# Kernel optimization log

Hardware: AMD Instinct MI355X
Metric: run time of the kernel (lower is better)

Reference implementation:

```python
import jax, jax.numpy as jnp
import numpy as np

SIGMA = 2.0
B, F, N = 4, 64, 4096


def setup_inputs() -> dict:
    key = jax.random.key(0)
    emb_in = jax.random.normal(key, (B, F, N), dtype=jnp.float32)
    adj_in = jnp.zeros((B, N, N), dtype=jnp.float32)  # unused by the module, kept for interface fidelity
    return {"adj_in": adj_in, "emb_in": emb_in}


def reference(adj_in, emb_in):
    # torch .std() is over all elements with Bessel's correction (ddof=1)
    std = jnp.std(emb_in, ddof=1)
    coord = emb_in / std  # [B, F, N]
    fmap = coord.shape[1]
    # mean_f (a-b)^2 = (|a|^2 + |b|^2 - 2 a.b) / F  -- GEMM trick, avoids [B,F,N,N]
    sq = jnp.sum(coord * coord, axis=1)              # [B, N]
    inner = jnp.einsum('bfn,bfm->bnm', coord, coord)  # [B, N, N]
    d2 = (sq[:, :, None] + sq[:, None, :] - 2.0 * inner) / fmap
    d2 = jnp.maximum(d2, 0.0)  # guard tiny negatives from cancellation
    return jnp.exp(-d2 / SIGMA)
```

## Files before the change

### kernel.cpp

```cpp
#include <hip/hip_runtime.h>
#include <hip/hip_bf16.h>

namespace {

constexpr int kB = 4, kF = 64, kN = 4096;
constexpr int kM = kB * kF * kN;

typedef __attribute__((ext_vector_type(8))) short bf16x8;
typedef __attribute__((ext_vector_type(4))) float f32x4;

__device__ __forceinline__ void wave_red2(float& s, float& q) {
#pragma unroll
  for (int o = 32; o > 0; o >>= 1) {
    s += __shfl_down(s, o, 64);
    q += __shfl_down(q, o, 64);
  }
}

__global__ void k_reduce1(const float* __restrict__ emb, float* __restrict__ part) {
  int t = blockIdx.x * blockDim.x + threadIdx.x;
  float4 v = reinterpret_cast<const float4*>(emb)[t];
  float s = v.x + v.y + v.z + v.w;
  float q = v.x * v.x + v.y * v.y + v.z * v.z + v.w * v.w;
  wave_red2(s, q);
  __shared__ float ls[4], lq[4];
  int lane = threadIdx.x & 63, w = threadIdx.x >> 6;
  if (lane == 0) { ls[w] = s; lq[w] = q; }
  __syncthreads();
  if (threadIdx.x == 0) {
    s = ls[0] + ls[1] + ls[2] + ls[3];
    q = lq[0] + lq[1] + lq[2] + lq[3];
    part[blockIdx.x] = s;
    part[1024 + blockIdx.x] = q;
  }
}

__global__ __launch_bounds__(256) void k_convert(const float* __restrict__ emb,
                                                 const float* __restrict__ part,
                                                 unsigned short* __restrict__ coordT,
                                                 float* __restrict__ sq) {
  int t = threadIdx.x;
  float s = part[t] + part[t + 256] + part[t + 512] + part[t + 768];
  float q = part[1024 + t] + part[1280 + t] + part[1536 + t] + part[1792 + t];
  wave_red2(s, q);
  __shared__ float ls[4], lq[4];
  __shared__ float s_inv;
  int lane = t & 63, w = t >> 6;
  if (lane == 0) { ls[w] = s; lq[w] = q; }
  __syncthreads();
  if (t == 0) {
    s = ls[0] + ls[1] + ls[2] + ls[3];
    q = lq[0] + lq[1] + lq[2] + lq[3];
    float mean = s / (float)kM;
    float var = (q - s * mean) / (float)(kM - 1);
    s_inv = 1.0f / sqrtf(var);
  }
  __syncthreads();
  float inv_std = s_inv;

  int nl = t & 63, fq = t >> 6;
  int g = blockIdx.x * 64 + nl;
  int b = g >> 12, n = g & 4095;
  const float* src = emb + ((size_t)b * kF + fq * 16) * kN + n;
  alignas(16) unsigned short loc[16];
  float acc = 0.f;
#pragma unroll
  for (int f = 0; f < 16; f++) {
    float v = src[(size_t)f * kN] * inv_std;
    union { __hip_bfloat16 h; unsigned short u; } cv;
    cv.h = __float2bfloat16(v);
    loc[f] = cv.u;
    float vf = __bfloat162float(cv.h);
    acc += vf * vf;
  }
  bf16x8* dst = reinterpret_cast<bf16x8*>(coordT + (size_t)g * kF + fq * 16);
  dst[0] = reinterpret_cast<const bf16x8*>(loc)[0];
  dst[1] = reinterpret_cast<const bf16x8*>(loc)[1];

  __shared__ float pacc[4][64];
  pacc[fq][nl] = acc;
  __syncthreads();
  if (fq == 0) sq[g] = pacc[0][nl] + pacc[1][nl] + pacc[2][nl] + pacc[3][nl];
}

__global__ __launch_bounds__(256, 2) void k_gemm_exp(const unsigned short* __restrict__ coordT,
                                                     const float* __restrict__ sq,
                                                     float* __restrict__ out) {
  int b = blockIdx.z;
  int wid = threadIdx.x >> 6;
  int lane = threadIdx.x & 63;
  int lhi = lane >> 4, llo = lane & 15;
  int i0 = blockIdx.y * 128 + (wid >> 1) * 64;
  int j0 = blockIdx.x * 128 + (wid & 1) * 64;
  const unsigned short* base = coordT + (size_t)b * kN * kF;

  bf16x8 af[4][2], bfr[4][2];
#pragma unroll
  for (int m = 0; m < 4; m++) {
    const unsigned short* p = base + (size_t)(i0 + m * 16 + llo) * kF + lhi * 8;
    af[m][0] = *reinterpret_cast<const bf16x8*>(p);
    af[m][1] = *reinterpret_cast<const bf16x8*>(p + 32);
  }
#pragma unroll
  for (int n = 0; n < 4; n++) {
    const unsigned short* p = base + (size_t)(j0 + n * 16 + llo) * kF + lhi * 8;
    bfr[n][0] = *reinterpret_cast<const bf16x8*>(p);
    bfr[n][1] = *reinterpret_cast<const bf16x8*>(p + 32);
  }

  f32x4 acc[4][4] = {};
#pragma unroll
  for (int kk = 0; kk < 2; kk++)
#pragma unroll
    for (int m = 0; m < 4; m++)
#pragma unroll
      for (int n = 0; n < 4; n++)
        acc[m][n] = __builtin_amdgcn_mfma_f32_16x16x32_bf16(af[m][kk], bfr[n][kk], acc[m][n], 0, 0, 0);

  const float* sqb = sq + (size_t)b * kN;
  float si[4][4];
#pragma unroll
  for (int m = 0; m < 4; m++) {
    f32x4 tv = *reinterpret_cast<const f32x4*>(&sqb[i0 + m * 16 + lhi * 4]);
    si[m][0] = tv[0]; si[m][1] = tv[1]; si[m][2] = tv[2]; si[m][3] = tv[3];
  }
  float sj[4];
#pragma unroll
  for (int n = 0; n < 4; n++) sj[n] = sqb[j0 + n * 16 + llo];

  constexpr float kC = -0.011271055f;
  float* ob = out + (size_t)b * kN * kN;
#pragma unroll
  for (int n = 0; n < 4; n++) {
    float* rp = ob + (size_t)(j0 + n * 16 + llo) * kN + i0 + (lhi << 2);
#pragma unroll
    for (int m = 0; m < 4; m++) {
      f32x4 wv;
#pragma unroll
      for (int r = 0; r < 4; r++) {
        float raw = si[m][r] + sj[n] - 2.0f * acc[m][n][r];
        raw = fmaxf(raw, 0.0f);
        wv[r] = __builtin_amdgcn_exp2f(raw * kC);
      }
      *reinterpret_cast<f32x4*>(rp + m * 16) = wv;
    }
  }
}

}

extern "C" void kernel_launch(void* const* d_in, const int* in_sizes, int n_in,
                              void* d_out, int out_size, void* d_ws, size_t ws_size,
                              hipStream_t stream) {
  const float* emb = (const float*)d_in[1];
  float* out = (float*)d_out;

  float* part = (float*)d_ws;
  unsigned short* coordT = (unsigned short*)((char*)d_ws + 16384);
  float* sq = (float*)((char*)d_ws + 16384 + (size_t)kB * kN * kF * sizeof(unsigned short));

  k_reduce1<<<1024, 256, 0, stream>>>(emb, part);
  k_convert<<<(kB * kN) / 64, 256, 0, stream>>>(emb, part, coordT, sq);
  dim3 grid(kN / 128, kN / 128, kB);
  k_gemm_exp<<<grid, 256, 0, stream>>>(coordT, sq, out);
}
```

Before: 76.14 us.

## Retile GEMM-exp to 16x1024 strips and stage output through LDS

```diff
diff --git a/kernel.cpp b/kernel.cpp
--- a/kernel.cpp
+++ b/kernel.cpp
@@ -86,63 +86,63 @@
 __global__ __launch_bounds__(256, 2) void k_gemm_exp(const unsigned short* __restrict__ coordT,
                                                      const float* __restrict__ sq,
                                                      float* __restrict__ out) {
+  constexpr int kPitch = 1028;
+  __shared__ float lds[16 * kPitch];
+
   int b = blockIdx.z;
   int wid = threadIdx.x >> 6;
   int lane = threadIdx.x & 63;
   int lhi = lane >> 4, llo = lane & 15;
-  int i0 = blockIdx.y * 128 + (wid >> 1) * 64;
-  int j0 = blockIdx.x * 128 + (wid & 1) * 64;
+  int y0 = blockIdx.y * 16;
+  int x0 = blockIdx.x * 1024;
+  int xw = x0 + wid * 256;
   const unsigned short* base = coordT + (size_t)b * kN * kF;
+  const float* sqb = sq + (size_t)b * kN;
 
-  bf16x8 af[4][2], bfr[4][2];
+  bf16x8 bf0, bf1;
+  {
+    const unsigned short* p = base + (size_t)(y0 + llo) * kF + lhi * 8;
+    bf0 = *reinterpret_cast<const bf16x8*>(p);
+    bf1 = *reinterpret_cast<const bf16x8*>(p + 32);
+  }
+  float sj = sqb[y0 + llo];
+
+  f32x4 acc[16];
 #pragma unroll
-  for (int m = 0; m < 4; m++) {
-    const unsigned short* p = base + (size_t)(i0 + m * 16 + llo) * kF + lhi * 8;
-    af[m][0] = *reinterpret_cast<const bf16x8*>(p);
-    af[m][1] = *reinterpret_cast<const bf16x8*>(p + 32);
-  }
-#pragma unroll
-  for (int n = 0; n < 4; n++) {
-    const unsigned short* p = base + (size_t)(j0 + n * 16 + llo) * kF + lhi * 8;
-    bfr[n][0] = *reinterpret_cast<const bf16x8*>(p);
-    bfr[n][1] = *reinterpret_cast<const bf16x8*>(p + 32);
+  for (int m = 0; m < 16; m++) {
+    const unsigned short* p = base + (size_t)(xw + m * 16 + llo) * kF + lhi * 8;
+    bf16x8 a0 = *reinterpret_cast<const bf16x8*>(p);
+    bf16x8 a1 = *reinterpret_cast<const bf16x8*>(p + 32);
+    f32x4 z = {};
+    z = __builtin_amdgcn_mfma_f32_16x16x32_bf16(a0, bf0, z, 0, 0, 0);
+    acc[m] = __builtin_amdgcn_mfma_f32_16x16x32_bf16(a1, bf1, z, 0, 0, 0);
   }
 
-  f32x4 acc[4][4] = {};
+  constexpr float kC = -0.011271055f;
 #pragma unroll
-  for (int kk = 0; kk < 2; kk++)
+  for (int m = 0; m < 16; m++) {
+    f32x4 tv = *reinterpret_cast<const f32x4*>(&sqb[xw + m * 16 + lhi * 4]);
+    f32x4 wv;
 #pragma unroll
-    for (int m = 0; m < 4; m++)
+    for (int r = 0; r < 4; r++) {
+      float raw = tv[r] + sj - 2.0f * acc[m][r];
+      raw = fmaxf(raw, 0.0f);
+      wv[r] = __builtin_amdgcn_exp2f(raw * kC);
+    }
+    int xloc = wid * 256 + m * 16 + lhi * 4;
+    *reinterpret_cast<f32x4*>(&lds[llo * kPitch + xloc]) = wv;
+  }
+  __syncthreads();
+
+  float* ob = out + (size_t)b * kN * kN + (size_t)y0 * kN + x0;
 #pragma unroll
-      for (int n = 0; n < 4; n++)
-        acc[m][n] = __builtin_amdgcn_mfma_f32_16x16x32_bf16(af[m][kk], bfr[n][kk], acc[m][n], 0, 0, 0);
-
-  const float* sqb = sq + (size_t)b * kN;
-  float si[4][4];
+  for (int p = 0; p < 4; p++) {
+    int yloc = wid * 4 + p;
+    float* rp = ob + (size_t)yloc * kN;
 #pragma unroll
-  for (int m = 0; m < 4; m++) {
-    f32x4 tv = *reinterpret_cast<const f32x4*>(&sqb[i0 + m * 16 + lhi * 4]);
-    si[m][0] = tv[0]; si[m][1] = tv[1]; si[m][2] = tv[2]; si[m][3] = tv[3];
-  }
-  float sj[4];
-#pragma unroll
-  for (int n = 0; n < 4; n++) sj[n] = sqb[j0 + n * 16 + llo];
-
-  constexpr float kC = -0.011271055f;
-  float* ob = out + (size_t)b * kN * kN;
-#pragma unroll
-  for (int n = 0; n < 4; n++) {
-    float* rp = ob + (size_t)(j0 + n * 16 + llo) * kN + i0 + (lhi << 2);
-#pragma unroll
-    for (int m = 0; m < 4; m++) {
-      f32x4 wv;
-#pragma unroll
-      for (int r = 0; r < 4; r++) {
-        float raw = si[m][r] + sj[n] - 2.0f * acc[m][n][r];
-        raw = fmaxf(raw, 0.0f);
-        wv[r] = __builtin_amdgcn_exp2f(raw * kC);
-      }
-      *reinterpret_cast<f32x4*>(rp + m * 16) = wv;
+    for (int c = 0; c < 4; c++) {
+      f32x4 v = *reinterpret_cast<const f32x4*>(&lds[yloc * kPitch + c * 256 + lane * 4]);
+      *reinterpret_cast<f32x4*>(rp + c * 256 + lane * 4) = v;
     }
   }
 }
@@ -161,6 +161,6 @@
 
   k_reduce1<<<1024, 256, 0, stream>>>(emb, part);
   k_convert<<<(kB * kN) / 64, 256, 0, stream>>>(emb, part, coordT, sq);
-  dim3 grid(kN / 128, kN / 128, kB);
+  dim3 grid(kN / 1024, kN / 16, kB);
   k_gemm_exp<<<grid, 256, 0, stream>>>(coordT, sq, out);
 }
```

After: 102.9 us. +35.1%, slower.
